# Kernel tuning notes

Hardware: AMD Instinct MI355X
Metric: run time of the kernel (lower is better)

Reference implementation:

```python
import jax, jax.numpy as jnp
import numpy as np

N, H, W, C = 8, 64, 64, 256
GC = 8            # channels per group (gc)
G = C // GC       # groups = 32
K = 3             # deformable kernel size
KK = K * K
DK = 3            # depthwise kernel size for offset/mask branch


def setup_inputs() -> dict:
    key = jax.random.key(0)
    ks = jax.random.split(key, 6)
    s = 0.02
    return {
        "x": jax.random.normal(ks[0], (N, H, W, C), jnp.float32),
        "dw_w": jax.random.normal(ks[1], (DK, DK, 1, C), jnp.float32) * s,
        "dw_b": jnp.zeros((C,), jnp.float32),
        "om_w": jax.random.normal(ks[2], (C, G * KK * 3), jnp.float32) * s,
        "om_b": jnp.zeros((G * KK * 3,), jnp.float32),
        "vp_w": jax.random.normal(ks[3], (C, C), jnp.float32) * s,
        "vp_b": jnp.zeros((C,), jnp.float32),
        "op_w": jax.random.normal(ks[4], (C, C), jnp.float32) * s,  # output_bias=False
    }


def _dcnv4(x, dw_w, dw_b, om_w, om_b, vp_w, vp_b, op_w):
    n, h, w, c = x.shape
    # --- offset/mask branch: depthwise conv then pointwise linear ---
    xdw = jax.lax.conv_general_dilated(
        x, dw_w, window_strides=(1, 1), padding="SAME",
        dimension_numbers=("NHWC", "HWIO", "NHWC"), feature_group_count=c) + dw_b
    om = (xdw @ om_w + om_b).reshape(n, h, w, G, KK * 3)
    offset = om[..., : 2 * KK].reshape(n, h, w, G, KK, 2)  # (dx, dy) per point
    mask = om[..., 2 * KK :]                                # [n,h,w,G,KK], raw (no softmax in v4)

    # --- value projection ---
    value = (x @ vp_w + vp_b).reshape(n, h, w, G, GC)

    # --- sampling locations: pixel + kernel-grid point + learned offset ---
    kg = (jnp.arange(K) - (K - 1) // 2).astype(jnp.float32)
    ky = jnp.repeat(kg, K)   # [KK]
    kx = jnp.tile(kg, K)     # [KK]
    base_y = jnp.arange(h, dtype=jnp.float32).reshape(1, h, 1, 1, 1)
    base_x = jnp.arange(w, dtype=jnp.float32).reshape(1, 1, w, 1, 1)
    py = base_y + ky + offset[..., 1]  # [n,h,w,G,KK]
    px = base_x + kx + offset[..., 0]

    y0 = jnp.floor(py)
    x0 = jnp.floor(px)
    ty = py - y0
    tx = px - x0

    n_idx = jnp.arange(n).reshape(n, 1, 1, 1, 1)
    g_idx = jnp.arange(G).reshape(1, 1, 1, G, 1)

    def gather(yi, xi):
        valid = (yi >= 0) & (yi <= h - 1) & (xi >= 0) & (xi <= w - 1)
        yc = jnp.clip(yi, 0, h - 1).astype(jnp.int32)
        xc = jnp.clip(xi, 0, w - 1).astype(jnp.int32)
        v = value[n_idx, yc, xc, g_idx]          # [n,h,w,G,KK,GC]
        return v * valid[..., None].astype(value.dtype)

    v00 = gather(y0, x0)
    v01 = gather(y0, x0 + 1)
    v10 = gather(y0 + 1, x0)
    v11 = gather(y0 + 1, x0 + 1)

    sampled = ((1 - ty) * (1 - tx))[..., None] * v00 \
            + ((1 - ty) * tx)[..., None] * v01 \
            + (ty * (1 - tx))[..., None] * v10 \
            + (ty * tx)[..., None] * v11        # [n,h,w,G,KK,GC]

    out = jnp.einsum("nhwgkc,nhwgk->nhwgc", sampled, mask).reshape(n, h, w, c)
    return out @ op_w                            # output proj, no bias


def reference(x, dw_w, dw_b, om_w, om_b, vp_w, vp_b, op_w):
    return _dcnv4(x, dw_w, dw_b, om_w, om_b, vp_w, vp_b, op_w)
```

## Files before the change

kernel.cpp:

```cpp
#include <hip/hip_runtime.h>


typedef __bf16 bf16_t;
typedef bf16_t bf16x8 __attribute__((ext_vector_type(8)));
typedef bf16_t bf16x4 __attribute__((ext_vector_type(4)));
typedef float f32x4 __attribute__((ext_vector_type(4)));

namespace {
constexpr int NN = 8, HH = 64, WW = 64, CC = 256;
constexpr int G = 32, GC = 8, OMD = 864;
constexpr int NPIX = NN * HH * WW;
}

__device__ __forceinline__ size_t fragIdx(int row, int c) {
  return ((size_t)(row >> 4) * 4096) + ((c >> 5) * 512) + (((c >> 3) & 3) * 128) +
         ((row & 15) * 8) + (c & 7);
}

__global__ __launch_bounds__(256) void convert_weights_kernel(
    const float* __restrict__ om_w, const float* __restrict__ vp_w,
    const float* __restrict__ op_w, bf16_t* __restrict__ om_wF,
    bf16_t* __restrict__ vp_wF, bf16_t* __restrict__ op_wF) {
  __shared__ float s_t[64][65];
  const int b = blockIdx.x, t = threadIdx.x;
  const float* src;
  bf16_t* dst;
  int ld, ncols, nt, kt;
  if (b < 56) {
    src = om_w; dst = om_wF; ld = OMD; ncols = OMD; kt = b / 14; nt = b % 14;
  } else if (b < 72) {
    const int i = b - 56;
    src = vp_w; dst = vp_wF; ld = CC; ncols = CC; kt = i >> 2; nt = i & 3;
  } else {
    const int i = b - 72;
    src = op_w; dst = op_wF; ld = CC; ncols = CC; kt = i >> 2; nt = i & 3;
  }
  const int nl = t & 63, kh = t >> 6;
  const int n = nt * 64 + nl;
#pragma unroll
  for (int i = 0; i < 16; ++i) {
    const int kl = kh * 16 + i;
    s_t[kl][nl] = (n < ncols) ? src[(size_t)(kt * 64 + kl) * ld + n] : 0.0f;
  }
  __syncthreads();
  const int lane = t & 63, kq = lane >> 4, n15 = lane & 15, n16 = t >> 6;
#pragma unroll
  for (int it = 0; it < 2; ++it) {
    bf16x8 v;
#pragma unroll
    for (int j = 0; j < 8; ++j) v[j] = (bf16_t)s_t[it * 32 + kq * 8 + j][n16 * 16 + n15];
    const size_t off = (size_t)(nt * 4 + n16) * 4096 + (size_t)(kt * 2 + it) * 512 +
                       kq * 128 + n15 * 8;
    *(bf16x8*)(dst + off) = v;
  }
}

__global__ __launch_bounds__(512, 4) void dwconv_value_kernel(
    const float* __restrict__ x, const float* __restrict__ dw_w,
    const float* __restrict__ dw_b, const bf16_t* __restrict__ vp_wF,
    const float* __restrict__ vp_b, bf16_t* __restrict__ xdwF,
    bf16_t* __restrict__ value_g) {
  __shared__ bf16_t s_xf[64 * 256];

  const int t = threadIdx.x;
  const int row = blockIdx.x;
  const int y = row & 63;
  const int img = row >> 6;

  {
    const int cq = (t & 63) * 4;
    const int seg = t >> 6;
    const bool up = (y > 0), dn = (y < HH - 1);
    const float* xrow = x + (size_t)row * WW * CC + cq;

    const float4 bias = *(const float4*)&dw_b[cq];
    float4 dw[9];
#pragma unroll
    for (int i = 0; i < 9; ++i) dw[i] = *(const float4*)&dw_w[(size_t)i * CC + cq];

    const float4 zero = make_float4(0.f, 0.f, 0.f, 0.f);
    auto loadcol = [&](int xx, float4 c[3]) {
      if (xx < 0 || xx >= WW) { c[0] = c[1] = c[2] = zero; return; }
      c[0] = up ? *(const float4*)(xrow + ((size_t)xx - WW) * CC) : zero;
      c[1] = *(const float4*)(xrow + (size_t)xx * CC);
      c[2] = dn ? *(const float4*)(xrow + ((size_t)xx + WW) * CC) : zero;
    };

    const int x0 = seg * 8;
    float4 cm[3], cc[3], cp[3];
    loadcol(x0 - 1, cm);
    loadcol(x0, cc);

    for (int xx = x0; xx < x0 + 8; ++xx) {
      loadcol(xx + 1, cp);
      float4 a = bias;
#pragma unroll
      for (int r = 0; r < 3; ++r) {
        const float4 w0 = dw[r * 3 + 0], w1 = dw[r * 3 + 1], w2 = dw[r * 3 + 2];
        a.x = fmaf(cm[r].x, w0.x, fmaf(cc[r].x, w1.x, fmaf(cp[r].x, w2.x, a.x)));
        a.y = fmaf(cm[r].y, w0.y, fmaf(cc[r].y, w1.y, fmaf(cp[r].y, w2.y, a.y)));
        a.z = fmaf(cm[r].z, w0.z, fmaf(cc[r].z, w1.z, fmaf(cp[r].z, w2.z, a.z)));
        a.w = fmaf(cm[r].w, w0.w, fmaf(cc[r].w, w1.w, fmaf(cp[r].w, w2.w, a.w)));
      }
      const int pix = row * WW + xx;
      bf16x4 av, cv;
      av[0] = (bf16_t)a.x; av[1] = (bf16_t)a.y; av[2] = (bf16_t)a.z; av[3] = (bf16_t)a.w;
      cv[0] = (bf16_t)cc[1].x; cv[1] = (bf16_t)cc[1].y;
      cv[2] = (bf16_t)cc[1].z; cv[3] = (bf16_t)cc[1].w;
      *(bf16x4*)&xdwF[fragIdx(pix, cq)] = av;
      const int lf = (xx >> 4) * 4096 + ((cq >> 5) * 512) + (((cq >> 3) & 3) * 128) +
                     ((xx & 15) * 8) + (cq & 7);
      *(bf16x4*)&s_xf[lf] = cv;
#pragma unroll
      for (int r = 0; r < 3; ++r) { cm[r] = cc[r]; cc[r] = cp[r]; }
    }
  }
  __syncthreads();

  {
    const int lane = t & 63;
    const int wave = t >> 6;
    const int mq = wave >> 1;
    const int nh = wave & 1;
    const int m = lane & 15;
    const int kq = lane >> 4;

    const bf16_t* Ap = s_xf + mq * 4096 + lane * 8;
    const bf16_t* Bp = vp_wF + (size_t)(nh * 8) * 4096 + lane * 8;

    f32x4 acc[8] = {};
#pragma unroll
    for (int ks = 0; ks < 8; ++ks) {
      const bf16x8 a = *(const bf16x8*)(Ap + ks * 512);
#pragma unroll
      for (int i = 0; i < 8; ++i) {
        const bf16x8 b = *(const bf16x8*)(Bp + (size_t)i * 4096 + ks * 512);
        acc[i] = __builtin_amdgcn_mfma_f32_16x16x32_bf16(a, b, acc[i], 0, 0, 0);
      }
    }

#pragma unroll
    for (int i = 0; i < 8; ++i) {
      const int n = (nh * 8 + i) * 16 + m;
      const float bs = vp_b[n];
      const int g = n >> 3, c = n & 7;
      bf16_t* plane = value_g + ((size_t)(img * G + g) << 15) + c;
#pragma unroll
      for (int r = 0; r < 4; ++r) {
        const int pl = mq * 16 + kq * 4 + r;
        const int pin = y * 64 + pl;
        plane[(size_t)pin * GC] = (bf16_t)(acc[i][r] + bs);
      }
    }
  }
}

__global__ __launch_bounds__(512, 4) void om_sample_mfma_kernel(
    const bf16_t* __restrict__ xdwF, const bf16_t* __restrict__ om_wF,
    const float* __restrict__ om_b, const bf16_t* __restrict__ value_g,
    bf16_t* __restrict__ sampledF) {
  __shared__ bf16_t s_om[32 * 1024];

  const int lane = threadIdx.x & 63;
  const int wave = threadIdx.x >> 6;
  const int pix0 = blockIdx.x * 32;

  {
    const int m = lane & 15;
    const int kq = lane >> 4;
    const bf16_t* Ap = xdwF + (size_t)(blockIdx.x * 2) * 4096 + lane * 8;
    const bf16_t* Bp = om_wF + (size_t)(wave * 7) * 4096 + lane * 8;
    f32x4 acc[2][7] = {};
#pragma unroll
    for (int ks = 0; ks < 8; ++ks) {
      const bf16x8 a0 = *(const bf16x8*)(Ap + ks * 512);
      const bf16x8 a1 = *(const bf16x8*)(Ap + 4096 + ks * 512);
#pragma unroll
      for (int i = 0; i < 7; ++i) {
        const bf16x8 b = *(const bf16x8*)(Bp + (size_t)i * 4096 + ks * 512);
        acc[0][i] = __builtin_amdgcn_mfma_f32_16x16x32_bf16(a0, b, acc[0][i], 0, 0, 0);
        acc[1][i] = __builtin_amdgcn_mfma_f32_16x16x32_bf16(a1, b, acc[1][i], 0, 0, 0);
      }
    }
#pragma unroll
    for (int i = 0; i < 7; ++i) {
      const int nt = wave * 7 + i;
      if (nt < 54) {
        const int n = nt * 16 + m;
        const float bs = om_b[n];
        const int g = n / 27;
        const int j = n - 27 * g;
        const int cj = j >> 3, jl = j & 7;
#pragma unroll
        for (int mt2 = 0; mt2 < 2; ++mt2)
#pragma unroll
          for (int r = 0; r < 4; ++r) {
            const int p = mt2 * 16 + kq * 4 + r;
            s_om[p * 1024 + (((g * 4 + cj + p) & 127) * 8) + jl] =
                (bf16_t)(acc[mt2][i][r] + bs);
          }
      }
    }
  }
  __syncthreads();

  const int gl = lane >> 4;
  const int g = wave * 4 + gl;
#pragma unroll
  for (int iter = 0; iter < 2; ++iter) {
    const int p = (lane & 15) + iter * 16;
    const int pix = pix0 + p;
    const int xw = pix & 63;
    const int y = (pix >> 6) & 63;
    const int img = pix >> 12;
    const bf16_t* plane = value_g + ((size_t)(img * G + g) << 15);

    const bf16_t* omp = &s_om[p * 1024];
    const int g4p = g * 4 + p;
    const bf16x8 o0 = *(const bf16x8*)(omp + ((g4p + 0) & 127) * 8);
    const bf16x8 o1 = *(const bf16x8*)(omp + ((g4p + 1) & 127) * 8);
    const bf16x8 o2 = *(const bf16x8*)(omp + ((g4p + 2) & 127) * 8);
    const bf16x8 o3 = *(const bf16x8*)(omp + ((g4p + 3) & 127) * 8);
    float arr[27];
#pragma unroll
    for (int j = 0; j < 8; ++j) {
      arr[j] = (float)o0[j];
      arr[8 + j] = (float)o1[j];
      arr[16 + j] = (float)o2[j];
    }
#pragma unroll
    for (int j = 0; j < 3; ++j) arr[24 + j] = (float)o3[j];

    float acc[GC];
#pragma unroll
    for (int c = 0; c < GC; ++c) acc[c] = 0.0f;

#pragma unroll
    for (int k = 0; k < 9; ++k) {
      const float px = (float)(xw + (k % 3) - 1) + arr[2 * k];
      const float py = (float)(y + (k / 3) - 1) + arr[2 * k + 1];
      const float mk = arr[18 + k];
      const float x0f = floorf(px), y0f = floorf(py);
      const float tx = px - x0f, ty = py - y0f;
      const int ix = (int)x0f, iy = (int)y0f;

      const float vx0 = (ix >= 0 && ix < WW) ? 1.0f : 0.0f;
      const float vx1 = (ix + 1 >= 0 && ix + 1 < WW) ? 1.0f : 0.0f;
      const float vy0 = (iy >= 0 && iy < HH) ? 1.0f : 0.0f;
      const float vy1 = (iy + 1 >= 0 && iy + 1 < HH) ? 1.0f : 0.0f;
      const int ix0 = min(max(ix, 0), WW - 1);
      const int ix1 = min(max(ix + 1, 0), WW - 1);
      const int iy0 = min(max(iy, 0), HH - 1);
      const int iy1 = min(max(iy + 1, 0), HH - 1);

      const bf16x8 v00 = *(const bf16x8*)(plane + (size_t)(iy0 * WW + ix0) * GC);
      const bf16x8 v01 = *(const bf16x8*)(plane + (size_t)(iy0 * WW + ix1) * GC);
      const bf16x8 v10 = *(const bf16x8*)(plane + (size_t)(iy1 * WW + ix0) * GC);
      const bf16x8 v11 = *(const bf16x8*)(plane + (size_t)(iy1 * WW + ix1) * GC);

      const float w00 = mk * (1.0f - ty) * (1.0f - tx) * vy0 * vx0;
      const float w01 = mk * (1.0f - ty) * tx * vy0 * vx1;
      const float w10 = mk * ty * (1.0f - tx) * vy1 * vx0;
      const float w11 = mk * ty * tx * vy1 * vx1;

#pragma unroll
      for (int c = 0; c < GC; ++c) {
        float s = acc[c];
        s = fmaf(w00, (float)v00[c], s);
        s = fmaf(w01, (float)v01[c], s);
        s = fmaf(w10, (float)v10[c], s);
        s = fmaf(w11, (float)v11[c], s);
        acc[c] = s;
      }
    }

    bf16x8 sv;
#pragma unroll
    for (int c = 0; c < GC; ++c) sv[c] = (bf16_t)acc[c];
    *(bf16x8*)(sampledF + (size_t)(blockIdx.x * 2 + iter) * 4096 + wave * 512 +
               lane * 8) = sv;
  }
}

__global__ __launch_bounds__(512, 4) void out_gemm_kernel(
    const bf16_t* __restrict__ AF, const bf16_t* __restrict__ BF,
    float* __restrict__ out) {
  const int lane = threadIdx.x & 63;
  const int wave = threadIdx.x >> 6;
  const int mq = wave >> 1;
  const int nh = wave & 1;
  const int mt = blockIdx.x * 4 + mq;
  const int m = lane & 15;
  const int kq = lane >> 4;

  const bf16_t* Ap = AF + (size_t)mt * 4096 + lane * 8;
  const bf16_t* Bp = BF + (size_t)(nh * 8) * 4096 + lane * 8;

  f32x4 acc[8] = {};
#pragma unroll
  for (int ks = 0; ks < 8; ++ks) {
    const bf16x8 a = *(const bf16x8*)(Ap + ks * 512);
#pragma unroll
    for (int i = 0; i < 8; ++i) {
      const bf16x8 b = *(const bf16x8*)(Bp + (size_t)i * 4096 + ks * 512);
      acc[i] = __builtin_amdgcn_mfma_f32_16x16x32_bf16(a, b, acc[i], 0, 0, 0);
    }
  }

#pragma unroll
  for (int i = 0; i < 8; ++i) {
    const int n = (nh * 8 + i) * 16 + m;
#pragma unroll
    for (int r = 0; r < 4; ++r) {
      const int pix = mt * 16 + kq * 4 + r;
      out[(size_t)pix * CC + n] = acc[i][r];
    }
  }
}

extern "C" void kernel_launch(void* const* d_in, const int* in_sizes, int n_in,
                              void* d_out, int out_size, void* d_ws, size_t ws_size,
                              hipStream_t stream) {
  const float* x = (const float*)d_in[0];
  const float* dw_w = (const float*)d_in[1];
  const float* dw_b = (const float*)d_in[2];
  const float* om_w = (const float*)d_in[3];
  const float* om_b = (const float*)d_in[4];
  const float* vp_w = (const float*)d_in[5];
  const float* vp_b = (const float*)d_in[6];
  const float* op_w = (const float*)d_in[7];
  float* out = (float*)d_out;

  char* ws = (char*)d_ws;
  bf16_t* value_g = (bf16_t*)ws;
  bf16_t* xdwF = (bf16_t*)(ws + 16777216);
  bf16_t* sampledF = (bf16_t*)(ws + 33554432);
  bf16_t* om_wF = (bf16_t*)(ws + 50331648);
  bf16_t* vp_wF = (bf16_t*)(ws + 50790400);
  bf16_t* op_wF = (bf16_t*)(ws + 50921472);

  convert_weights_kernel<<<88, 256, 0, stream>>>(om_w, vp_w, op_w,
                                                 om_wF, vp_wF, op_wF);
  dwconv_value_kernel<<<NN * HH, 512, 0, stream>>>(x, dw_w, dw_b, vp_wF, vp_b,
                                                   xdwF, value_g);
  om_sample_mfma_kernel<<<NPIX / 32, 512, 0, stream>>>(xdwF, om_wF, om_b,
                                                       value_g, sampledF);
  out_gemm_kernel<<<NPIX / 64, 512, 0, stream>>>(sampledF, op_wF, out);
}
```

Measured before the change: 214.6 us.

## Split offset GEMM from sampling and stage value planes in LDS with zero halo

```diff
diff --git a/kernel.cpp b/kernel.cpp
--- a/kernel.cpp
+++ b/kernel.cpp
@@ -155,72 +155,115 @@
   }
 }
 
-__global__ __launch_bounds__(512, 4) void om_sample_mfma_kernel(
+__global__ __launch_bounds__(512, 2) void om_gemm_kernel(
     const bf16_t* __restrict__ xdwF, const bf16_t* __restrict__ om_wF,
-    const float* __restrict__ om_b, const bf16_t* __restrict__ value_g,
+    const float* __restrict__ om_b, bf16_t* __restrict__ omP) {
+  __shared__ bf16_t s_a[64 * 256];
+
+  const int t = threadIdx.x;
+  const int lane = t & 63;
+  const int wave = t >> 6;
+
+  {
+    const bf16_t* src = xdwF + (size_t)blockIdx.x * 16384;
+#pragma unroll
+    for (int i = 0; i < 4; ++i) {
+      const int idx = (i * 512 + t) * 8;
+      *(bf16x8*)(s_a + idx) = *(const bf16x8*)(src + idx);
+    }
+  }
+  __syncthreads();
+
+  const int m = lane & 15;
+  const int kq = lane >> 4;
+  const bf16_t* Bp = om_wF + (size_t)(wave * 7) * 4096 + lane * 8;
+
+  f32x4 acc[4][7] = {};
+#pragma unroll
+  for (int ks = 0; ks < 8; ++ks) {
+    bf16x8 a[4];
+#pragma unroll
+    for (int mt = 0; mt < 4; ++mt)
+      a[mt] = *(const bf16x8*)(s_a + mt * 4096 + ks * 512 + lane * 8);
+#pragma unroll
+    for (int i = 0; i < 7; ++i) {
+      const bf16x8 b = *(const bf16x8*)(Bp + (size_t)i * 4096 + ks * 512);
+#pragma unroll
+      for (int mt = 0; mt < 4; ++mt)
+        acc[mt][i] =
+            __builtin_amdgcn_mfma_f32_16x16x32_bf16(a[mt], b, acc[mt][i], 0, 0, 0);
+    }
+  }
+
+  const int pix0 = blockIdx.x * 64;
+  const int img = pix0 >> 12;
+  const int pin0 = pix0 & 4095;
+#pragma unroll
+  for (int i = 0; i < 7; ++i) {
+    const int nt = wave * 7 + i;
+    if (nt < 54) {
+      const int n = nt * 16 + m;
+      const float bs = om_b[n];
+      const int g = n / 27;
+      const int j = n - g * 27;
+      bf16_t* dst = omP + ((size_t)(img * G + g) * 4096 + pin0) * 32 + j;
+#pragma unroll
+      for (int mt = 0; mt < 4; ++mt)
+#pragma unroll
+        for (int r = 0; r < 4; ++r) {
+          const int pl = mt * 16 + kq * 4 + r;
+          dst[(size_t)pl * 32] = (bf16_t)(acc[mt][i][r] + bs);
+        }
+    }
+  }
+}
+
+__global__ __launch_bounds__(512, 2) void sample_kernel(
+    const bf16_t* __restrict__ omP, const bf16_t* __restrict__ value_g,
     bf16_t* __restrict__ sampledF) {
-  __shared__ bf16_t s_om[32 * 1024];
-
-  const int lane = threadIdx.x & 63;
-  const int wave = threadIdx.x >> 6;
-  const int pix0 = blockIdx.x * 32;
+  __shared__ bf16x8 s_v[66 * 66];
+
+  const int t = threadIdx.x;
+  const int b = blockIdx.x;
+  const int img = b >> 6;
+  const int g = (b >> 1) & 31;
+  const int half = b & 1;
 
   {
-    const int m = lane & 15;
-    const int kq = lane >> 4;
-    const bf16_t* Ap = xdwF + (size_t)(blockIdx.x * 2) * 4096 + lane * 8;
-    const bf16_t* Bp = om_wF + (size_t)(wave * 7) * 4096 + lane * 8;
-    f32x4 acc[2][7] = {};
-#pragma unroll
-    for (int ks = 0; ks < 8; ++ks) {
-      const bf16x8 a0 = *(const bf16x8*)(Ap + ks * 512);
-      const bf16x8 a1 = *(const bf16x8*)(Ap + 4096 + ks * 512);
-#pragma unroll
-      for (int i = 0; i < 7; ++i) {
-        const bf16x8 b = *(const bf16x8*)(Bp + (size_t)i * 4096 + ks * 512);
-        acc[0][i] = __builtin_amdgcn_mfma_f32_16x16x32_bf16(a0, b, acc[0][i], 0, 0, 0);
-        acc[1][i] = __builtin_amdgcn_mfma_f32_16x16x32_bf16(a1, b, acc[1][i], 0, 0, 0);
-      }
-    }
-#pragma unroll
-    for (int i = 0; i < 7; ++i) {
-      const int nt = wave * 7 + i;
-      if (nt < 54) {
-        const int n = nt * 16 + m;
-        const float bs = om_b[n];
-        const int g = n / 27;
-        const int j = n - 27 * g;
-        const int cj = j >> 3, jl = j & 7;
-#pragma unroll
-        for (int mt2 = 0; mt2 < 2; ++mt2)
-#pragma unroll
-          for (int r = 0; r < 4; ++r) {
-            const int p = mt2 * 16 + kq * 4 + r;
-            s_om[p * 1024 + (((g * 4 + cj + p) & 127) * 8) + jl] =
-                (bf16_t)(acc[mt2][i][r] + bs);
-          }
-      }
+    const bf16x8 zv = {};
+    for (int i = t; i < 260; i += 512) {
+      int Y, X;
+      if (i < 66)       { Y = 0;            X = i; }
+      else if (i < 132) { Y = 65;           X = i - 66; }
+      else if (i < 196) { Y = i - 132 + 1;  X = 0; }
+      else              { Y = i - 196 + 1;  X = 65; }
+      s_v[Y * 66 + X] = zv;
+    }
+    const bf16x8* plane = (const bf16x8*)(value_g + ((size_t)(img * G + g) << 15));
+#pragma unroll
+    for (int i = 0; i < 8; ++i) {
+      const int c = i * 512 + t;
+      const int yy = c >> 6, xx = c & 63;
+      s_v[(yy + 1) * 66 + (xx + 1)] = plane[c];
     }
   }
   __syncthreads();
 
-  const int gl = lane >> 4;
-  const int g = wave * 4 + gl;
-#pragma unroll
-  for (int iter = 0; iter < 2; ++iter) {
-    const int p = (lane & 15) + iter * 16;
-    const int pix = pix0 + p;
-    const int xw = pix & 63;
-    const int y = (pix >> 6) & 63;
-    const int img = pix >> 12;
-    const bf16_t* plane = value_g + ((size_t)(img * G + g) << 15);
-
-    const bf16_t* omp = &s_om[p * 1024];
-    const int g4p = g * 4 + p;
-    const bf16x8 o0 = *(const bf16x8*)(omp + ((g4p + 0) & 127) * 8);
-    const bf16x8 o1 = *(const bf16x8*)(omp + ((g4p + 1) & 127) * 8);
-    const bf16x8 o2 = *(const bf16x8*)(omp + ((g4p + 2) & 127) * 8);
-    const bf16x8 o3 = *(const bf16x8*)(omp + ((g4p + 3) & 127) * 8);
+  const bf16_t* omBase =
+      omP + ((size_t)(img * G + g) * 4096 + (size_t)half * 2048) * 32;
+
+#pragma unroll
+  for (int it = 0; it < 4; ++it) {
+    const int pl = it * 512 + t;
+    const int px = half * 2048 + pl;
+    const int xw = px & 63;
+    const int y = px >> 6;
+
+    const bf16_t* op = omBase + (size_t)pl * 32;
+    const bf16x8 o0 = *(const bf16x8*)(op + 0);
+    const bf16x8 o1 = *(const bf16x8*)(op + 8);
+    const bf16x8 o2 = *(const bf16x8*)(op + 16);
+    const bf16x8 o3 = *(const bf16x8*)(op + 24);
     float arr[27];
 #pragma unroll
     for (int j = 0; j < 8; ++j) {
@@ -237,31 +280,27 @@
 
 #pragma unroll
     for (int k = 0; k < 9; ++k) {
-      const float px = (float)(xw + (k % 3) - 1) + arr[2 * k];
-      const float py = (float)(y + (k / 3) - 1) + arr[2 * k + 1];
+      const float pxf = (float)(xw + (k % 3) - 1) + arr[2 * k];
+      const float pyf = (float)(y + (k / 3) - 1) + arr[2 * k + 1];
       const float mk = arr[18 + k];
-      const float x0f = floorf(px), y0f = floorf(py);
-      const float tx = px - x0f, ty = py - y0f;
+      const float x0f = floorf(pxf), y0f = floorf(pyf);
+      const float tx = pxf - x0f, ty = pyf - y0f;
       const int ix = (int)x0f, iy = (int)y0f;
 
-      const float vx0 = (ix >= 0 && ix < WW) ? 1.0f : 0.0f;
-      const float vx1 = (ix + 1 >= 0 && ix + 1 < WW) ? 1.0f : 0.0f;
-      const float vy0 = (iy >= 0 && iy < HH) ? 1.0f : 0.0f;
-      const float vy1 = (iy + 1 >= 0 && iy + 1 < HH) ? 1.0f : 0.0f;
-      const int ix0 = min(max(ix, 0), WW - 1);
-      const int ix1 = min(max(ix + 1, 0), WW - 1);
-      const int iy0 = min(max(iy, 0), HH - 1);
-      const int iy1 = min(max(iy + 1, 0), HH - 1);
-
-      const bf16x8 v00 = *(const bf16x8*)(plane + (size_t)(iy0 * WW + ix0) * GC);
-      const bf16x8 v01 = *(const bf16x8*)(plane + (size_t)(iy0 * WW + ix1) * GC);
-      const bf16x8 v10 = *(const bf16x8*)(plane + (size_t)(iy1 * WW + ix0) * GC);
-      const bf16x8 v11 = *(const bf16x8*)(plane + (size_t)(iy1 * WW + ix1) * GC);
-
-      const float w00 = mk * (1.0f - ty) * (1.0f - tx) * vy0 * vx0;
-      const float w01 = mk * (1.0f - ty) * tx * vy0 * vx1;
-      const float w10 = mk * ty * (1.0f - tx) * vy1 * vx0;
-      const float w11 = mk * ty * tx * vy1 * vx1;
+      const int iX0 = min(max(ix, -1), 64) + 1;
+      const int iX1 = min(max(ix + 1, -1), 64) + 1;
+      const int iY0 = min(max(iy, -1), 64) + 1;
+      const int iY1 = min(max(iy + 1, -1), 64) + 1;
+
+      const bf16x8 v00 = s_v[iY0 * 66 + iX0];
+      const bf16x8 v01 = s_v[iY0 * 66 + iX1];
+      const bf16x8 v10 = s_v[iY1 * 66 + iX0];
+      const bf16x8 v11 = s_v[iY1 * 66 + iX1];
+
+      const float w00 = mk * (1.0f - ty) * (1.0f - tx);
+      const float w01 = mk * (1.0f - ty) * tx;
+      const float w10 = mk * ty * (1.0f - tx);
+      const float w11 = mk * ty * tx;
 
 #pragma unroll
       for (int c = 0; c < GC; ++c) {
@@ -277,8 +316,7 @@
     bf16x8 sv;
 #pragma unroll
     for (int c = 0; c < GC; ++c) sv[c] = (bf16_t)acc[c];
-    *(bf16x8*)(sampledF + (size_t)(blockIdx.x * 2 + iter) * 4096 + wave * 512 +
-               lane * 8) = sv;
+    *(bf16x8*)(sampledF + fragIdx(img * 4096 + px, g * 8)) = sv;
   }
 }
 
@@ -332,18 +370,19 @@
   float* out = (float*)d_out;
 
   char* ws = (char*)d_ws;
-  bf16_t* value_g = (bf16_t*)ws;
-  bf16_t* xdwF = (bf16_t*)(ws + 16777216);
-  bf16_t* sampledF = (bf16_t*)(ws + 33554432);
-  bf16_t* om_wF = (bf16_t*)(ws + 50331648);
-  bf16_t* vp_wF = (bf16_t*)(ws + 50790400);
-  bf16_t* op_wF = (bf16_t*)(ws + 50921472);
+  bf16_t* omP = (bf16_t*)ws;
+  bf16_t* value_g = (bf16_t*)(ws + 67108864);
+  bf16_t* xdwF = (bf16_t*)(ws + 83886080);
+  bf16_t* sampledF = xdwF;
+  bf16_t* om_wF = (bf16_t*)(ws + 100663296);
+  bf16_t* vp_wF = (bf16_t*)(ws + 101122048);
+  bf16_t* op_wF = (bf16_t*)(ws + 101253120);
 
   convert_weights_kernel<<<88, 256, 0, stream>>>(om_w, vp_w, op_w,
                                                  om_wF, vp_wF, op_wF);
   dwconv_value_kernel<<<NN * HH, 512, 0, stream>>>(x, dw_w, dw_b, vp_wF, vp_b,
                                                    xdwF, value_g);
-  om_sample_mfma_kernel<<<NPIX / 32, 512, 0, stream>>>(xdwF, om_wF, om_b,
-                                                       value_g, sampledF);
+  om_gemm_kernel<<<NPIX / 64, 512, 0, stream>>>(xdwF, om_wF, om_b, omP);
+  sample_kernel<<<NPIX / 64, 512, 0, stream>>>(omP, value_g, sampledF);
   out_gemm_kernel<<<NPIX / 64, 512, 0, stream>>>(sampledF, op_wF, out);
 }
```

Result: slower. 230.3 us (+7.3%).
